# Kernel tuning notes

Measured on AMD Instinct MI355X. Metric: run time of the kernel, lower is better.

Reference implementation:

```python
import jax, jax.numpy as jnp
import numpy as np

N_NODES = 100_000
N_EDGES = 1_600_000
N_GRAPHS = 200
N_IN, N_HID, N_OUT, N_LAYERS = 4, 64, 2, 4


def _ln(x, g, b, eps=1e-5):
    mu = jnp.mean(x, -1, keepdims=True)
    xc = x - mu
    var = jnp.mean(xc * xc, -1, keepdims=True)
    return xc * jax.lax.rsqrt(var + eps) * g + b


def _sage(x, src, dst, Wl, bl, Wr, n):
    # SAGEConv with MultiAggregation(['max','mean'], mode='cat'):
    # out = lin_l(concat(max_j x_j, mean_j x_j)) + lin_r(x)
    xj = x[src]  # [E, d] edge gather
    mx = jax.ops.segment_max(xj, dst, num_segments=n)
    mx = jnp.where(jnp.isneginf(mx), 0.0, mx)  # PyG scatter-max gives 0 for isolated nodes
    s = jax.ops.segment_sum(xj, dst, num_segments=n)
    cnt = jax.ops.segment_sum(jnp.ones((src.shape[0], 1), x.dtype), dst, num_segments=n)
    mean = s / jnp.maximum(cnt, 1.0)
    agg = jnp.concatenate([mx, mean], -1)  # [N, 2d], order = aggr list order
    return agg @ Wl + bl + x @ Wr


def setup_inputs():
    key = jax.random.key(0)
    ks = jax.random.split(key, 16)
    x = jax.random.normal(ks[0], (N_NODES, N_IN), jnp.float32)
    edge_index = jax.random.randint(ks[1], (2, N_EDGES), 0, N_NODES, dtype=jnp.int32)
    per = N_NODES // N_GRAPHS
    batch = jnp.repeat(jnp.arange(N_GRAPHS, dtype=jnp.int32), per)
    ptr = jnp.arange(N_GRAPHS + 1, dtype=jnp.int32) * per

    def w(k, shape, fan_in):
        return jax.random.normal(k, shape, jnp.float32) / np.sqrt(fan_in)

    inp = dict(x=x, edge_index=edge_index, batch=batch, ptr=ptr)
    inp["Wl0"] = w(ks[2], (2 * N_IN, N_HID), 2 * N_IN)
    inp["bl0"] = jnp.zeros((N_HID,), jnp.float32)
    inp["Wr0"] = w(ks[3], (N_IN, N_HID), N_IN)
    inp["Wl"] = w(ks[4], (N_LAYERS - 1, 2 * N_HID, N_HID), 2 * N_HID)
    inp["bl"] = jnp.zeros((N_LAYERS - 1, N_HID), jnp.float32)
    inp["Wr"] = w(ks[5], (N_LAYERS - 1, N_HID, N_HID), N_HID)
    inp["Wres"] = w(ks[6], (N_IN, N_HID), N_IN)
    inp["bres"] = jnp.zeros((N_HID,), jnp.float32)
    inp["ln_g"] = jnp.ones((N_LAYERS, N_HID), jnp.float32)
    inp["ln_b"] = jnp.zeros((N_LAYERS, N_HID), jnp.float32)
    inp["mlp_W1"] = w(ks[7], (N_HID, 4 * N_HID), N_HID)
    inp["mlp_b1"] = jnp.zeros((4 * N_HID,), jnp.float32)
    inp["mlp_g"] = jnp.ones((4 * N_HID,), jnp.float32)
    inp["mlp_bn"] = jnp.zeros((4 * N_HID,), jnp.float32)
    inp["mlp_W2"] = w(ks[8], (4 * N_HID, N_HID), 4 * N_HID)
    inp["mlp_b2"] = jnp.zeros((N_HID,), jnp.float32)
    ro_in = 3 * N_HID + N_IN
    inp["ro_W1"] = w(ks[9], (ro_in, 4 * N_HID), ro_in)
    inp["ro_b1"] = jnp.zeros((4 * N_HID,), jnp.float32)
    inp["ro_g"] = jnp.ones((4 * N_HID,), jnp.float32)
    inp["ro_bn"] = jnp.zeros((4 * N_HID,), jnp.float32)
    inp["ro_W2"] = w(ks[10], (4 * N_HID, 2 * N_OUT), 4 * N_HID)
    inp["ro_b2"] = jnp.zeros((2 * N_OUT,), jnp.float32)
    return inp


def reference(x, edge_index, batch, ptr, Wl0, bl0, Wr0, Wl, bl, Wr, Wres, bres,
              ln_g, ln_b, mlp_W1, mlp_b1, mlp_g, mlp_bn, mlp_W2, mlp_b2,
              ro_W1, ro_b1, ro_g, ro_bn, ro_W2, ro_b2):
    n = x.shape[0]
    ng = ptr.shape[0] - 1
    src, dst = edge_index[0], edge_index[1]

    x_res = x @ Wres + bres
    h = _sage(x, src, dst, Wl0, bl0, Wr0, n)
    h = jax.nn.silu(_ln(h, ln_g[0], ln_b[0]) + x_res)
    for i in range(Wl.shape[0]):  # n_layers - 1 structurally distinct layers
        h_res = h
        h = _sage(h, src, dst, Wl[i], bl[i], Wr[i], n)
        h = jax.nn.silu(_ln(h, ln_g[i + 1], ln_b[i + 1]) + h_res)

    h = jax.nn.silu(h @ mlp_W1 + mlp_b1)
    h = _ln(h, mlp_g, mlp_bn) @ mlp_W2 + mlp_b2

    # multi-pool readout over graphs
    s = jax.ops.segment_sum(h, batch, num_segments=ng)
    cnt = jax.ops.segment_sum(jnp.ones((n, 1), h.dtype), batch, num_segments=ng)
    mean = s / jnp.maximum(cnt, 1.0)
    mx = jax.ops.segment_max(h, batch, num_segments=ng)
    mx = jnp.where(jnp.isneginf(mx), 0.0, mx)
    root = x[ptr[:-1]]  # original features of each graph's root node
    o = jnp.concatenate([mean, mx, s, root], -1)  # [G, 3*n_hidden + n_in]
    o = jax.nn.silu(o @ ro_W1 + ro_b1)
    return _ln(o, ro_g, ro_bn) @ ro_W2 + ro_b2
```

## Files before the change

kernel.cpp:

```cpp
#include <hip/hip_runtime.h>
#include <math.h>

#define NEG_INF (-__builtin_inff())
#define BSHIFT 8
#define BCAP 6144
#define SK 200

typedef __attribute__((ext_vector_type(8))) short short8;
typedef __attribute__((ext_vector_type(4))) float f32x4;

__device__ __forceinline__ float rlane(float x, int l) {
    return __int_as_float(__builtin_amdgcn_readlane(__float_as_int(x), l));
}

__device__ __forceinline__ float silu_f(float y) {
    return y / (1.f + __expf(-y));
}

__device__ __forceinline__ unsigned short f2bh(float x) {
    unsigned int u = __float_as_uint(x);
    u += 0x7fffu + ((u >> 16) & 1u);
    return (unsigned short)(u >> 16);
}
__device__ __forceinline__ float bh2f(unsigned short h) {
    return __uint_as_float(((unsigned int)h) << 16);
}


__global__ __launch_bounds__(256)
void k_bhist(const int* __restrict__ ei, int* __restrict__ btot, int E, int NB) {
    __shared__ int lh[512];
    int t = threadIdx.x;
    lh[t] = 0; lh[t + 256] = 0;
    __syncthreads();
    int base = blockIdx.x * 8192;
    for (int i = t; i < 8192; i += 256) {
        int e = base + i;
        if (e < E) atomicAdd(&lh[ei[E + e] >> BSHIFT], 1);
    }
    __syncthreads();
    if (lh[t]) atomicAdd(&btot[t], lh[t]);
    if (t + 256 < NB && lh[t + 256]) atomicAdd(&btot[t + 256], lh[t + 256]);
}

__global__ __launch_bounds__(256)
void k_bscan(const int* __restrict__ btot, int* __restrict__ bbase,
             int* __restrict__ bcur, int NB, int E) {
    __shared__ int s[512];
    int t = threadIdx.x;
    int v0 = (t < NB) ? btot[t] : 0;
    int v1 = (t + 256 < NB) ? btot[t + 256] : 0;
    s[t] = v0; s[t + 256] = v1;
    __syncthreads();
    for (int st = 1; st < 512; st <<= 1) {
        int a0 = (t >= st) ? s[t - st] : 0;
        int a1 = (t + 256 >= st) ? s[t + 256 - st] : 0;
        __syncthreads();
        s[t] += a0; s[t + 256] += a1;
        __syncthreads();
    }
    if (t < NB)       { bbase[t] = s[t] - v0;             bcur[t] = s[t] - v0; }
    if (t + 256 < NB) { bbase[t + 256] = s[t + 256] - v1; bcur[t + 256] = s[t + 256] - v1; }
    if (t == 0) bbase[NB] = E;
}

__global__ __launch_bounds__(256)
void k_bscatter(const int* __restrict__ ei, int* __restrict__ bcur,
                int2* __restrict__ pairs, int E, int NB) {
    __shared__ int2 sp[8192];
    __shared__ int lh[512], lsc[512], lcur[512], gb[512];
    int t = threadIdx.x;
    lh[t] = 0; lh[t + 256] = 0; lcur[t] = 0; lcur[t + 256] = 0;
    __syncthreads();
    int base = blockIdx.x * 8192;
    for (int i = t; i < 8192; i += 256) {
        int e = base + i;
        if (e < E) atomicAdd(&lh[ei[E + e] >> BSHIFT], 1);
    }
    __syncthreads();
    lsc[t] = lh[t]; lsc[t + 256] = lh[t + 256];
    __syncthreads();
    for (int st = 1; st < 512; st <<= 1) {
        int a0 = (t >= st) ? lsc[t - st] : 0;
        int a1 = (t + 256 >= st) ? lsc[t + 256 - st] : 0;
        __syncthreads();
        lsc[t] += a0; lsc[t + 256] += a1;
        __syncthreads();
    }
    for (int i = t; i < 8192; i += 256) {
        int e = base + i;
        if (e < E) {
            int s = ei[e], d = ei[E + e];
            int b = d >> BSHIFT;
            int pos = lsc[b] - lh[b] + atomicAdd(&lcur[b], 1);
            sp[pos] = make_int2(s, d);
        }
    }
    __syncthreads();
    if (t < NB && lh[t]) gb[t] = atomicAdd(&bcur[t], lh[t]);
    if (t + 256 < NB && lh[t + 256]) gb[t + 256] = atomicAdd(&bcur[t + 256], lh[t + 256]);
    __syncthreads();
    int tot = lsc[511];
    for (int i = t; i < tot; i += 256) {
        int2 p = sp[i];
        int b = p.y >> BSHIFT;
        pairs[gb[b] + (i - (lsc[b] - lh[b]))] = p;
    }
}

__global__ __launch_bounds__(256)
void k_bcsr(const int2* __restrict__ pairs, const int* __restrict__ bbase,
            int* __restrict__ csr, int* __restrict__ off, int N, int NB, int E) {
    __shared__ int2 sp[BCAP];
    __shared__ int lh[256], lsc[256], lcur[256];
    int t = threadIdx.x;
    int b = blockIdx.x;
    int base = bbase[b];
    int m = bbase[b + 1] - base;
    int v0 = b << BSHIFT;
    lh[t] = 0; lcur[t] = 0;
    __syncthreads();
    bool fits = (m <= BCAP);
    for (int i = t; i < m; i += 256) {
        int2 p = pairs[base + i];
        if (fits) sp[i] = p;
        atomicAdd(&lh[p.y & 255], 1);
    }
    __syncthreads();
    int myv = lh[t];
    lsc[t] = myv;
    __syncthreads();
    for (int st = 1; st < 256; st <<= 1) {
        int a = (t >= st) ? lsc[t - st] : 0;
        __syncthreads();
        lsc[t] += a;
        __syncthreads();
    }
    int excl = lsc[t] - myv;
    __syncthreads();
    lsc[t] = excl;
    __syncthreads();
    int v = v0 + t;
    if (v < N) off[v] = base + excl;
    if (b == NB - 1 && t == 0) off[N] = E;
    for (int i = t; i < m; i += 256) {
        int2 p = fits ? sp[i] : pairs[base + i];
        int d = p.y & 255;
        int pos = lsc[d] + atomicAdd(&lcur[d], 1);
        csr[base + pos] = p.x;
    }
}


__global__ void k_prep(const float* __restrict__ mW1, const float* __restrict__ mg,
                       const float* __restrict__ mbn, const float* __restrict__ mW2,
                       const float* __restrict__ mb2,
                       const float* __restrict__ Wl, const float* __restrict__ Wr,
                       unsigned short* __restrict__ w1fh, unsigned short* __restrict__ w1fl,
                       unsigned short* __restrict__ w2fh, unsigned short* __restrict__ w2fl,
                       unsigned short* __restrict__ wsfh, unsigned short* __restrict__ wsfl,
                       float* __restrict__ k12)
{
    int b = blockIdx.x, t = threadIdx.x;
    if (b == 0) {
        for (int idx = t; idx < 2048; idx += 256) {
            int nt = idx >> 7, rem = idx & 127;
            int kc = rem >> 6, ln = rem & 63;
#pragma unroll
            for (int i = 0; i < 8; ++i) {
                int c = kc * 32 + (ln >> 4) * 8 + i;
                int j = nt * 16 + (ln & 15);
                float v = mW1[c * 256 + j];
                unsigned short hi = f2bh(v);
                w1fh[idx * 8 + i] = hi;
                w1fl[idx * 8 + i] = f2bh(v - bh2f(hi));
            }
        }
    } else if (b == 1) {
        for (int idx = t; idx < 2048; idx += 256) {
            int nt2 = idx >> 9, rem = idx & 511;
            int kc2 = rem >> 6, ln = rem & 63;
#pragma unroll
            for (int i = 0; i < 8; ++i) {
                int j = kc2 * 32 + (ln >> 4) * 8 + i;
                int o = nt2 * 16 + (ln & 15);
                float v = mg[j] * mW2[j * 64 + o];
                unsigned short hi = f2bh(v);
                w2fh[idx * 8 + i] = hi;
                w2fl[idx * 8 + i] = f2bh(v - bh2f(hi));
            }
        }
    } else if (b == 2 && t < 64) {
        float a1 = 0.f, a2 = 0.f;
        for (int j = 0; j < 256; ++j) {
            a1 += mbn[j] * mW2[j * 64 + t];
            a2 += mg[j]  * mW2[j * 64 + t];
        }
        k12[t] = a1 + mb2[t];
        k12[64 + t] = a2;
    } else if (b >= 3 && b < 6) {
        int l = b - 3;
        for (int idx = t; idx < 1536; idx += 256) {
            int tile = idx >> 6, ln = idx & 63;
            int nt = tile / 6, kc = tile % 6;
#pragma unroll
            for (int i = 0; i < 8; ++i) {
                int k = kc * 32 + (ln >> 4) * 8 + i;
                int o = nt * 16 + (ln & 15);
                float v = (k < 128) ? Wl[((l * 128) + k) * 64 + o]
                                    : Wr[((l * 64) + (k - 128)) * 64 + o];
                unsigned short hi = f2bh(v);
                wsfh[((l * 24 + tile) * 64 + ln) * 8 + i] = hi;
                wsfl[((l * 24 + tile) * 64 + ln) * 8 + i] = f2bh(v - bh2f(hi));
            }
        }
    }
}


__global__ __launch_bounds__(256, 4)
void k_layer0(const float* __restrict__ x, float* __restrict__ hout,
              const int* __restrict__ off, const int* __restrict__ csr,
              const float* __restrict__ Wl0, const float* __restrict__ bl0,
              const float* __restrict__ Wr0, const float* __restrict__ Wres,
              const float* __restrict__ bres, const float* __restrict__ lg,
              const float* __restrict__ lb, int N)
{
    __shared__ float sWl[512], sWr[256], sWres[256], sC[256];
    int t = threadIdx.x;
    sWl[t] = Wl0[t]; sWl[256 + t] = Wl0[256 + t];
    sWr[t] = Wr0[t];
    sWres[t] = Wres[t];
    if (t < 64) { sC[t] = bl0[t]; sC[64 + t] = bres[t]; sC[128 + t] = lg[t]; sC[192 + t] = lb[t]; }
    __syncthreads();
    int v = blockIdx.x * 256 + t;
    if (v >= N) return;
    const float4* X4 = reinterpret_cast<const float4*>(x);
    float4 xv = X4[v];
    int s0 = off[v], s1 = off[v + 1];
    float4 mx = {NEG_INF, NEG_INF, NEG_INF, NEG_INF};
    float4 sm = {0.f, 0.f, 0.f, 0.f};
    for (int e = s0; e < s1; e += 4) {
        int last = s1 - 1;
        int i0 = csr[e];
        int i1 = csr[min(e + 1, last)];
        int i2 = csr[min(e + 2, last)];
        int i3 = csr[min(e + 3, last)];
        float4 a0 = X4[i0], a1 = X4[i1], a2 = X4[i2], a3 = X4[i3];
        mx.x = fmaxf(fmaxf(fmaxf(mx.x, a0.x), fmaxf(a1.x, a2.x)), a3.x);
        mx.y = fmaxf(fmaxf(fmaxf(mx.y, a0.y), fmaxf(a1.y, a2.y)), a3.y);
        mx.z = fmaxf(fmaxf(fmaxf(mx.z, a0.z), fmaxf(a1.z, a2.z)), a3.z);
        mx.w = fmaxf(fmaxf(fmaxf(mx.w, a0.w), fmaxf(a1.w, a2.w)), a3.w);
        bool o1 = e + 1 < s1, o2 = e + 2 < s1, o3 = e + 3 < s1;
        sm.x += a0.x + (o1 ? a1.x : 0.f) + (o2 ? a2.x : 0.f) + (o3 ? a3.x : 0.f);
        sm.y += a0.y + (o1 ? a1.y : 0.f) + (o2 ? a2.y : 0.f) + (o3 ? a3.y : 0.f);
        sm.z += a0.z + (o1 ? a1.z : 0.f) + (o2 ? a2.z : 0.f) + (o3 ? a3.z : 0.f);
        sm.w += a0.w + (o1 ? a1.w : 0.f) + (o2 ? a2.w : 0.f) + (o3 ? a3.w : 0.f);
    }
    int deg = s1 - s0;
    if (deg == 0) { mx.x = 0.f; mx.y = 0.f; mx.z = 0.f; mx.w = 0.f; }
    float inv = 1.f / (float)max(deg, 1);
    float4 mn = {sm.x * inv, sm.y * inv, sm.z * inv, sm.w * inv};
    float a[64];
    float acc1 = 0.f, acc2 = 0.f;
#pragma unroll
    for (int k = 0; k < 64; ++k) {
        float tv = sC[k]
            + mx.x * sWl[k]       + mx.y * sWl[64 + k]  + mx.z * sWl[128 + k] + mx.w * sWl[192 + k]
            + mn.x * sWl[256 + k] + mn.y * sWl[320 + k] + mn.z * sWl[384 + k] + mn.w * sWl[448 + k]
            + xv.x * sWr[k]       + xv.y * sWr[64 + k]  + xv.z * sWr[128 + k] + xv.w * sWr[192 + k];
        a[k] = tv; acc1 += tv; acc2 += tv * tv;
    }
    float mu = acc1 * (1.f / 64.f);
    float var = acc2 * (1.f / 64.f) - mu * mu;
    float rs = rsqrtf(var + 1e-5f);
    float* orow = hout + (size_t)v * 64;
#pragma unroll
    for (int k = 0; k < 64; ++k) {
        float res = sC[64 + k] + xv.x * sWres[k] + xv.y * sWres[64 + k]
                  + xv.z * sWres[128 + k] + xv.w * sWres[192 + k];
        float y = (a[k] - mu) * rs * sC[128 + k] + sC[192 + k] + res;
        orow[k] = silu_f(y);
    }
}


__global__ __launch_bounds__(256, 8)
void k_agg(const float* __restrict__ hin, float* __restrict__ aggws,
           const int* __restrict__ off, const int* __restrict__ csr, int N)
{
    int lane = threadIdx.x & 63;
    int gw = (blockIdx.x * blockDim.x + threadIdx.x) >> 6;
    int nw = (gridDim.x * blockDim.x) >> 6;
    for (int v = gw; v < N; v += nw) {
        int s0 = off[v], s1 = off[v + 1];
        float mx = NEG_INF, sm = 0.f;
        for (int cb = s0; cb < s1; cb += 64) {
            int cdeg = min(64, s1 - cb);
            int idxv = csr[min(cb + lane, s1 - 1)];
            for (int b = 0; b < cdeg; b += 8) {
                float vv[8];
#pragma unroll
                for (int u = 0; u < 8; ++u) {
                    int iu = __builtin_amdgcn_readlane(idxv, b + u);
                    vv[u] = hin[((size_t)iu << 6) + lane];
                }
#pragma unroll
                for (int u = 0; u < 8; ++u) {
                    mx = fmaxf(mx, vv[u]);
                    sm += (b + u < cdeg) ? vv[u] : 0.f;
                }
            }
        }
        int deg = s1 - s0;
        if (deg == 0) mx = 0.f;
        float mean = sm / (float)max(deg, 1);
        aggws[((size_t)v << 7) + lane] = mx;
        aggws[((size_t)v << 7) + 64 + lane] = mean;
    }
}


__global__ __launch_bounds__(256, 2)
void k_smm_m(const float* __restrict__ aggws, const float* __restrict__ hin,
             float* __restrict__ hout,
             const unsigned short* __restrict__ wfh, const unsigned short* __restrict__ wfl,
             const float* __restrict__ bl, const float* __restrict__ lg,
             const float* __restrict__ lb, int N)
{
    __shared__ __align__(16) unsigned short shi[64 * SK];
    __shared__ __align__(16) unsigned short slo[64 * SK];
    int t = threadIdx.x;
    int lane = t & 63, w = t >> 6, quad = lane >> 4, l15 = lane & 15;

    {
        int row = t >> 2, seg = t & 3;
        int node = min(blockIdx.x * 64 + row, N - 1);
        const float4* ar = (const float4*)(aggws + ((size_t)node << 7));
        const float4* hr = (const float4*)(hin + ((size_t)node << 6));
        float v[48];
#pragma unroll
        for (int q = 0; q < 12; ++q) {
            int c = seg * 48 + q * 4;
            float4 f = (c < 128) ? ar[c >> 2] : hr[(c - 128) >> 2];
            v[q * 4] = f.x; v[q * 4 + 1] = f.y; v[q * 4 + 2] = f.z; v[q * 4 + 3] = f.w;
        }
#pragma unroll
        for (int g = 0; g < 6; ++g) {
            short8 ph, pl;
#pragma unroll
            for (int i = 0; i < 8; ++i) {
                float x = v[g * 8 + i];
                unsigned short hi = f2bh(x);
                ph[i] = (short)hi;
                pl[i] = (short)f2bh(x - bh2f(hi));
            }
            int idx = row * SK + seg * 48 + g * 8;
            *(short8*)(shi + idx) = ph;
            *(short8*)(slo + idx) = pl;
        }
    }
    __syncthreads();

    f32x4 acc[4];
#pragma unroll
    for (int nt = 0; nt < 4; ++nt) acc[nt] = (f32x4){0.f, 0.f, 0.f, 0.f};
#pragma unroll
    for (int kc = 0; kc < 6; ++kc) {
        int idx = (w * 16 + l15) * SK + kc * 32 + quad * 8;
        short8 ah = *(const short8*)(shi + idx);
        short8 al = *(const short8*)(slo + idx);
#pragma unroll
        for (int nt = 0; nt < 4; ++nt) {
            int fo = ((nt * 6 + kc) * 64 + lane) * 8;
            short8 bh_ = *(const short8*)(wfh + fo);
            short8 bl_ = *(const short8*)(wfl + fo);
            acc[nt] = __builtin_amdgcn_mfma_f32_16x16x32_bf16(ah, bh_, acc[nt], 0, 0, 0);
            acc[nt] = __builtin_amdgcn_mfma_f32_16x16x32_bf16(al, bh_, acc[nt], 0, 0, 0);
            acc[nt] = __builtin_amdgcn_mfma_f32_16x16x32_bf16(ah, bl_, acc[nt], 0, 0, 0);
        }
    }

    float blv[4], gv[4], bv[4];
#pragma unroll
    for (int nt = 0; nt < 4; ++nt) {
        int ch = nt * 16 + l15;
        blv[nt] = bl[ch]; gv[nt] = lg[ch]; bv[nt] = lb[ch];
    }
    float ps[4], pq[4];
#pragma unroll
    for (int r = 0; r < 4; ++r) { ps[r] = 0.f; pq[r] = 0.f; }
#pragma unroll
    for (int nt = 0; nt < 4; ++nt)
#pragma unroll
        for (int r = 0; r < 4; ++r) {
            float tv = acc[nt][r] + blv[nt];
            acc[nt][r] = tv;
            ps[r] += tv; pq[r] += tv * tv;
        }
#pragma unroll
    for (int r = 0; r < 4; ++r) {
        float a = ps[r], b = pq[r];
#pragma unroll
        for (int m = 1; m < 16; m <<= 1) {
            a += __shfl_xor(a, m, 64);
            b += __shfl_xor(b, m, 64);
        }
        ps[r] = a; pq[r] = b;
    }
#pragma unroll
    for (int r = 0; r < 4; ++r) {
        int node = blockIdx.x * 64 + w * 16 + quad * 4 + r;
        float mu = ps[r] * (1.f / 64.f);
        float var = pq[r] * (1.f / 64.f) - mu * mu;
        float rs = rsqrtf(var + 1e-5f);
        if (node < N) {
#pragma unroll
            for (int nt = 0; nt < 4; ++nt) {
                float hs = hin[(size_t)node * 64 + nt * 16 + l15];
                float y = (acc[nt][r] - mu) * rs * gv[nt] + bv[nt] + hs;
                hout[(size_t)node * 64 + nt * 16 + l15] = silu_f(y);
            }
        }
    }
}


__global__ __launch_bounds__(256, 2)
void k_mlpm(const float* __restrict__ hin, float* __restrict__ hout,
            const unsigned short* __restrict__ w1fh, const unsigned short* __restrict__ w1fl,
            const unsigned short* __restrict__ w2fh, const unsigned short* __restrict__ w2fl,
            const float* __restrict__ b1, const float* __restrict__ K12, int N)
{
    __shared__ __align__(16) char lds[70656];
    float* p1 = (float*)lds;
    float* p2 = (float*)(lds + 1024);
    unsigned short* hhi = (unsigned short*)(lds + 2048);
    unsigned short* hlo = (unsigned short*)(lds + 11264);
    unsigned int* spack = (unsigned int*)(lds + 2048);

    int t = threadIdx.x;
    int lane = t & 63, w = t >> 6, quad = lane >> 4, l15 = lane & 15;

    {
        int row = t >> 2, cq = (t & 3) * 16;
        int node0 = blockIdx.x * 64 + row;
        const float4* hr = (const float4*)(hin + (size_t)min(node0, N - 1) * 64 + cq);
        float v[16];
#pragma unroll
        for (int k = 0; k < 4; ++k) {
            float4 f = hr[k];
            v[4 * k] = f.x; v[4 * k + 1] = f.y; v[4 * k + 2] = f.z; v[4 * k + 3] = f.w;
        }
#pragma unroll
        for (int g = 0; g < 2; ++g) {
            short8 ph, pl;
#pragma unroll
            for (int i = 0; i < 8; ++i) {
                float x = v[g * 8 + i];
                unsigned short hi = f2bh(x);
                ph[i] = (short)hi;
                pl[i] = (short)f2bh(x - bh2f(hi));
            }
            int idx = row * 72 + cq + g * 8;
            *(short8*)(hhi + idx) = ph;
            *(short8*)(hlo + idx) = pl;
        }
    }
    __syncthreads();

    f32x4 acc[4][4];
#pragma unroll
    for (int mt = 0; mt < 4; ++mt)
#pragma unroll
        for (int nt = 0; nt < 4; ++nt)
            acc[mt][nt] = (f32x4){0.f, 0.f, 0.f, 0.f};
#pragma unroll
    for (int kc = 0; kc < 2; ++kc) {
        short8 ah[4], al[4];
#pragma unroll
        for (int mt = 0; mt < 4; ++mt) {
            int idx = (mt * 16 + l15) * 72 + kc * 32 + quad * 8;
            ah[mt] = *(const short8*)(hhi + idx);
            al[mt] = *(const short8*)(hlo + idx);
        }
#pragma unroll
        for (int nt = 0; nt < 4; ++nt) {
            int fo = (((w * 4 + nt) * 2 + kc) * 64 + lane) * 8;
            short8 bh_ = *(const short8*)(w1fh + fo);
            short8 bl_ = *(const short8*)(w1fl + fo);
#pragma unroll
            for (int mt = 0; mt < 4; ++mt) {
                acc[mt][nt] = __builtin_amdgcn_mfma_f32_16x16x32_bf16(ah[mt], bh_, acc[mt][nt], 0, 0, 0);
                acc[mt][nt] = __builtin_amdgcn_mfma_f32_16x16x32_bf16(al[mt], bh_, acc[mt][nt], 0, 0, 0);
                acc[mt][nt] = __builtin_amdgcn_mfma_f32_16x16x32_bf16(ah[mt], bl_, acc[mt][nt], 0, 0, 0);
            }
        }
    }

    float b1v[4];
#pragma unroll
    for (int nt = 0; nt < 4; ++nt) b1v[nt] = b1[(w * 4 + nt) * 16 + l15];
    float psum[4][4], psq[4][4];
#pragma unroll
    for (int mt = 0; mt < 4; ++mt)
#pragma unroll
        for (int r = 0; r < 4; ++r) { psum[mt][r] = 0.f; psq[mt][r] = 0.f; }
#pragma unroll
    for (int mt = 0; mt < 4; ++mt)
#pragma unroll
        for (int nt = 0; nt < 4; ++nt)
#pragma unroll
            for (int r = 0; r < 4; ++r) {
                float sv = silu_f(acc[mt][nt][r] + b1v[nt]);
                acc[mt][nt][r] = sv;
                psum[mt][r] += sv;
                psq[mt][r] += sv * sv;
            }
#pragma unroll
    for (int mt = 0; mt < 4; ++mt)
#pragma unroll
        for (int r = 0; r < 4; ++r) {
            float a = psum[mt][r], b = psq[mt][r];
#pragma unroll
            for (int m = 1; m < 16; m <<= 1) {
                a += __shfl_xor(a, m, 64);
                b += __shfl_xor(b, m, 64);
            }
            psum[mt][r] = a; psq[mt][r] = b;
        }
    if (l15 == 0) {
#pragma unroll
        for (int mt = 0; mt < 4; ++mt)
#pragma unroll
            for (int r = 0; r < 4; ++r) {
                int nl = mt * 16 + quad * 4 + r;
                p1[w * 64 + nl] = psum[mt][r];
                p2[w * 64 + nl] = psq[mt][r];
            }
    }
    __syncthreads();

#pragma unroll
    for (int mt = 0; mt < 4; ++mt)
#pragma unroll
        for (int nt = 0; nt < 4; ++nt)
#pragma unroll
            for (int r = 0; r < 4; ++r) {
                float sv = acc[mt][nt][r];
                unsigned short hi = f2bh(sv);
                unsigned short lo = f2bh(sv - bh2f(hi));
                spack[(mt * 16 + quad * 4 + r) * 268 + (w * 4 + nt) * 16 + l15] =
                    (((unsigned int)hi) << 16) | (unsigned int)lo;
            }
    __syncthreads();

    f32x4 acc2[4];
#pragma unroll
    for (int nt2 = 0; nt2 < 4; ++nt2) acc2[nt2] = (f32x4){0.f, 0.f, 0.f, 0.f};
#pragma unroll
    for (int kc2 = 0; kc2 < 8; ++kc2) {
        int base = (w * 16 + l15) * 268 + kc2 * 32 + quad * 8;
        uint4 q0 = *(const uint4*)(spack + base);
        uint4 q1 = *(const uint4*)(spack + base + 4);
        unsigned int vv[8] = {q0.x, q0.y, q0.z, q0.w, q1.x, q1.y, q1.z, q1.w};
        short8 ah, al;
#pragma unroll
        for (int i = 0; i < 8; ++i) {
            ah[i] = (short)(vv[i] >> 16);
            al[i] = (short)(vv[i] & 0xffffu);
        }
#pragma unroll
        for (int nt2 = 0; nt2 < 4; ++nt2) {
            int fo = ((nt2 * 8 + kc2) * 64 + lane) * 8;
            short8 bh_ = *(const short8*)(w2fh + fo);
            short8 bl_ = *(const short8*)(w2fl + fo);
            acc2[nt2] = __builtin_amdgcn_mfma_f32_16x16x32_bf16(ah, bh_, acc2[nt2], 0, 0, 0);
            acc2[nt2] = __builtin_amdgcn_mfma_f32_16x16x32_bf16(al, bh_, acc2[nt2], 0, 0, 0);
            acc2[nt2] = __builtin_amdgcn_mfma_f32_16x16x32_bf16(ah, bl_, acc2[nt2], 0, 0, 0);
        }
    }

    float k1v[4], k2v[4];
#pragma unroll
    for (int nt2 = 0; nt2 < 4; ++nt2) {
        k1v[nt2] = K12[nt2 * 16 + l15];
        k2v[nt2] = K12[64 + nt2 * 16 + l15];
    }
#pragma unroll
    for (int r = 0; r < 4; ++r) {
        int nl = w * 16 + quad * 4 + r;
        float s1 = p1[nl] + p1[64 + nl] + p1[128 + nl] + p1[192 + nl];
        float s2 = p2[nl] + p2[64 + nl] + p2[128 + nl] + p2[192 + nl];
        float mu = s1 * (1.f / 256.f);
        float var = s2 * (1.f / 256.f) - mu * mu;
        float rs = rsqrtf(var + 1e-5f);
        float rm = rs * mu;
        int node = blockIdx.x * 64 + nl;
        if (node < N) {
#pragma unroll
            for (int nt2 = 0; nt2 < 4; ++nt2)
                hout[(size_t)node * 64 + nt2 * 16 + l15] =
                    rs * acc2[nt2][r] + k1v[nt2] - rm * k2v[nt2];
        }
    }
}


__global__ __launch_bounds__(256, 2)
void k_readout(const float* __restrict__ h2, const float* __restrict__ x,
               const int* __restrict__ ptr,
               const float* __restrict__ W1, const float* __restrict__ b1,
               const float* __restrict__ lg, const float* __restrict__ lb,
               const float* __restrict__ W2, const float* __restrict__ b2,
               float* __restrict__ out)
{
    __shared__ float f[196];
    __shared__ float sred[4][64];
    __shared__ float mred[4][64];
    __shared__ float lred[8];
    __shared__ float pr[4][4];
    int t = threadIdx.x, lane = t & 63, w = t >> 6;
    int g = blockIdx.x;
    int s0 = ptr[g], s1 = ptr[g + 1];
    float sm = 0.f, mx = NEG_INF;
    for (int r = s0 + w; r < s1; r += 4) {
        float v = h2[(size_t)r * 64 + lane];
        sm += v; mx = fmaxf(mx, v);
    }
    sred[w][lane] = sm; mred[w][lane] = mx;
    __syncthreads();
    if (w == 0) {
        float ssum = sred[0][lane] + sred[1][lane] + sred[2][lane] + sred[3][lane];
        float smax = fmaxf(fmaxf(mred[0][lane], mred[1][lane]),
                           fmaxf(mred[2][lane], mred[3][lane]));
        int cnt = s1 - s0;
        if (cnt == 0) smax = 0.f;
        f[lane] = ssum / (float)max(cnt, 1);
        f[64 + lane] = smax;
        f[128 + lane] = ssum;
    }
    if (t < 4) f[192 + t] = x[(size_t)s0 * 4 + t];
    __syncthreads();
    float o = b1[t];
    for (int c = 0; c < 196; ++c) o += f[c] * W1[c * 256 + t];
    o = silu_f(o);
    float s = o, s2v = o * o;
#pragma unroll
    for (int m = 1; m < 64; m <<= 1) { s += __shfl_xor(s, m, 64); s2v += __shfl_xor(s2v, m, 64); }
    if (lane == 0) { lred[w] = s; lred[4 + w] = s2v; }
    __syncthreads();
    float tot = lred[0] + lred[1] + lred[2] + lred[3];
    float tot2 = lred[4] + lred[5] + lred[6] + lred[7];
    float mu = tot * (1.f / 256.f);
    float var = tot2 * (1.f / 256.f) - mu * mu;
    float u = (o - mu) * rsqrtf(var + 1e-5f) * lg[t] + lb[t];
    float4 w2r = reinterpret_cast<const float4*>(W2)[t];
    float p0 = u * w2r.x, p1 = u * w2r.y, p2 = u * w2r.z, p3 = u * w2r.w;
#pragma unroll
    for (int m = 1; m < 64; m <<= 1) {
        p0 += __shfl_xor(p0, m, 64); p1 += __shfl_xor(p1, m, 64);
        p2 += __shfl_xor(p2, m, 64); p3 += __shfl_xor(p3, m, 64);
    }
    if (lane == 0) { pr[w][0] = p0; pr[w][1] = p1; pr[w][2] = p2; pr[w][3] = p3; }
    __syncthreads();
    if (t < 4) out[g * 4 + t] = pr[0][t] + pr[1][t] + pr[2][t] + pr[3][t] + b2[t];
}


extern "C" void kernel_launch(void* const* d_in, const int* in_sizes, int n_in,
                              void* d_out, int out_size, void* d_ws, size_t ws_size,
                              hipStream_t stream)
{
    const float* x    = (const float*)d_in[0];
    const int*   ei   = (const int*)d_in[1];
    const int*   ptr  = (const int*)d_in[3];
    const float* Wl0  = (const float*)d_in[4];
    const float* bl0  = (const float*)d_in[5];
    const float* Wr0  = (const float*)d_in[6];
    const float* Wl   = (const float*)d_in[7];
    const float* bl   = (const float*)d_in[8];
    const float* Wr   = (const float*)d_in[9];
    const float* Wres = (const float*)d_in[10];
    const float* bres = (const float*)d_in[11];
    const float* lng  = (const float*)d_in[12];
    const float* lnb  = (const float*)d_in[13];
    const float* mW1  = (const float*)d_in[14];
    const float* mb1  = (const float*)d_in[15];
    const float* mg   = (const float*)d_in[16];
    const float* mbn  = (const float*)d_in[17];
    const float* mW2  = (const float*)d_in[18];
    const float* mb2  = (const float*)d_in[19];
    const float* rW1  = (const float*)d_in[20];
    const float* rb1  = (const float*)d_in[21];
    const float* rg   = (const float*)d_in[22];
    const float* rbn  = (const float*)d_in[23];
    const float* rW2  = (const float*)d_in[24];
    const float* rb2  = (const float*)d_in[25];
    float* out = (float*)d_out;

    int N = in_sizes[0] / 4;
    int E = in_sizes[1] / 2;
    int NG = in_sizes[3] - 1;
    int nchunk = (N + 255) / 256;
    int nblkm  = (N + 63) / 64;
    int NB     = (N + 255) >> BSHIFT;
    int nbh    = (E + 8191) / 8192;

    char* ws = (char*)d_ws;
    size_t o = 0;
    auto alloc = [&](size_t bytes) -> void* {
        void* p = ws + o;
        o += (bytes + 255) & ~(size_t)255;
        return p;
    };
    int*   off   = (int*)alloc((size_t)(N + 1) * 4);
    int*   btot  = (int*)alloc((size_t)NB * 4);
    int*   bbase = (int*)alloc((size_t)(NB + 1) * 4);
    int*   bcur  = (int*)alloc((size_t)NB * 4);
    int*   csr   = (int*)alloc((size_t)E * 4);
    int2*  pairs = (int2*)alloc((size_t)E * 8);
    float* ha    = (float*)alloc((size_t)N * 64 * 4);
    float* hb    = (float*)alloc((size_t)N * 64 * 4);
    float* aggws = (float*)alloc((size_t)N * 128 * 4);
    unsigned short* w1fh = (unsigned short*)alloc(16384 * 2);
    unsigned short* w1fl = (unsigned short*)alloc(16384 * 2);
    unsigned short* w2fh = (unsigned short*)alloc(16384 * 2);
    unsigned short* w2fl = (unsigned short*)alloc(16384 * 2);
    unsigned short* wsfh = (unsigned short*)alloc(36864 * 2);
    unsigned short* wsfl = (unsigned short*)alloc(36864 * 2);
    float* k12   = (float*)alloc(128 * 4);

    hipMemsetAsync(btot, 0, (size_t)NB * 4, stream);
    k_prep<<<6, 256, 0, stream>>>(mW1, mg, mbn, mW2, mb2, Wl, Wr,
                                  w1fh, w1fl, w2fh, w2fl, wsfh, wsfl, k12);
    k_bhist<<<nbh, 256, 0, stream>>>(ei, btot, E, NB);
    k_bscan<<<1, 256, 0, stream>>>(btot, bbase, bcur, NB, E);
    k_bscatter<<<nbh, 256, 0, stream>>>(ei, bcur, pairs, E, NB);
    k_bcsr<<<NB, 256, 0, stream>>>(pairs, bbase, csr, off, N, NB, E);

    k_layer0<<<nchunk, 256, 0, stream>>>(x, ha, off, csr, Wl0, bl0, Wr0, Wres, bres, lng, lnb, N);

    k_agg<<<2048, 256, 0, stream>>>(ha, aggws, off, csr, N);
    k_smm_m<<<nblkm, 256, 0, stream>>>(aggws, ha, hb, wsfh,               wsfl,               bl,       lng + 64,  lnb + 64,  N);
    k_agg<<<2048, 256, 0, stream>>>(hb, aggws, off, csr, N);
    k_smm_m<<<nblkm, 256, 0, stream>>>(aggws, hb, ha, wsfh + 24 * 64 * 8, wsfl + 24 * 64 * 8, bl + 64,  lng + 128, lnb + 128, N);
    k_agg<<<2048, 256, 0, stream>>>(ha, aggws, off, csr, N);
    k_smm_m<<<nblkm, 256, 0, stream>>>(aggws, ha, hb, wsfh + 48 * 64 * 8, wsfl + 48 * 64 * 8, bl + 128, lng + 192, lnb + 192, N);

    k_mlpm<<<nblkm, 256, 0, stream>>>(hb, ha, w1fh, w1fl, w2fh, w2fl, mb1, k12, N);
    k_readout<<<NG, 256, 0, stream>>>(ha, x, ptr, rW1, rb1, rg, rbn, rW2, rb2, out);
}
```

Before: 609.1 us.

## Load SAGE GEMM operands directly to registers, widen gather unroll, halve bucket chunks

The SAGE dense kernel no longer stages the split-bf16 A tiles in LDS. Each wave now loads its 16 rows straight from global memory into MFMA operand registers, which removes the shared-memory round trip and the block barrier and allows higher occupancy. The aggregation gather is unrolled to 16 loads per step and drops the per-element predicate. To keep the mean correct, it subtracts the padded duplicates of the last neighbor afterwards, which can add a small floating-point cancellation error. The edge bucketing chunk is also halved so that more blocks are launched and less LDS is used per block.

```diff
diff --git a/kernel.cpp b/kernel.cpp
--- a/kernel.cpp
+++ b/kernel.cpp
@@ -4,14 +4,10 @@
 #define NEG_INF (-__builtin_inff())
 #define BSHIFT 8
 #define BCAP 6144
-#define SK 200
+#define CH 4096
 
 typedef __attribute__((ext_vector_type(8))) short short8;
 typedef __attribute__((ext_vector_type(4))) float f32x4;
-
-__device__ __forceinline__ float rlane(float x, int l) {
-    return __int_as_float(__builtin_amdgcn_readlane(__float_as_int(x), l));
-}
 
 __device__ __forceinline__ float silu_f(float y) {
     return y / (1.f + __expf(-y));
@@ -33,8 +29,8 @@
     int t = threadIdx.x;
     lh[t] = 0; lh[t + 256] = 0;
     __syncthreads();
-    int base = blockIdx.x * 8192;
-    for (int i = t; i < 8192; i += 256) {
+    int base = blockIdx.x * CH;
+    for (int i = t; i < CH; i += 256) {
         int e = base + i;
         if (e < E) atomicAdd(&lh[ei[E + e] >> BSHIFT], 1);
     }
@@ -67,13 +63,13 @@
 __global__ __launch_bounds__(256)
 void k_bscatter(const int* __restrict__ ei, int* __restrict__ bcur,
                 int2* __restrict__ pairs, int E, int NB) {
-    __shared__ int2 sp[8192];
+    __shared__ int2 sp[CH];
     __shared__ int lh[512], lsc[512], lcur[512], gb[512];
     int t = threadIdx.x;
     lh[t] = 0; lh[t + 256] = 0; lcur[t] = 0; lcur[t + 256] = 0;
     __syncthreads();
-    int base = blockIdx.x * 8192;
-    for (int i = t; i < 8192; i += 256) {
+    int base = blockIdx.x * CH;
+    for (int i = t; i < CH; i += 256) {
         int e = base + i;
         if (e < E) atomicAdd(&lh[ei[E + e] >> BSHIFT], 1);
     }
@@ -87,7 +83,7 @@
         lsc[t] += a0; lsc[t + 256] += a1;
         __syncthreads();
     }
-    for (int i = t; i < 8192; i += 256) {
+    for (int i = t; i < CH; i += 256) {
         int e = base + i;
         if (e < E) {
             int s = ei[e], d = ei[E + e];
@@ -294,90 +290,79 @@
     int nw = (gridDim.x * blockDim.x) >> 6;
     for (int v = gw; v < N; v += nw) {
         int s0 = off[v], s1 = off[v + 1];
+        int deg = s1 - s0;
         float mx = NEG_INF, sm = 0.f;
+        int npad = 0;
         for (int cb = s0; cb < s1; cb += 64) {
             int cdeg = min(64, s1 - cb);
             int idxv = csr[min(cb + lane, s1 - 1)];
-            for (int b = 0; b < cdeg; b += 8) {
-                float vv[8];
-#pragma unroll
-                for (int u = 0; u < 8; ++u) {
+            for (int b = 0; b < cdeg; b += 16) {
+                float vv[16];
+#pragma unroll
+                for (int u = 0; u < 16; ++u) {
                     int iu = __builtin_amdgcn_readlane(idxv, b + u);
                     vv[u] = hin[((size_t)iu << 6) + lane];
                 }
 #pragma unroll
-                for (int u = 0; u < 8; ++u) {
-                    mx = fmaxf(mx, vv[u]);
-                    sm += (b + u < cdeg) ? vv[u] : 0.f;
-                }
-            }
-        }
-        int deg = s1 - s0;
-        if (deg == 0) mx = 0.f;
-        float mean = sm / (float)max(deg, 1);
+                for (int u = 0; u < 16; ++u) { mx = fmaxf(mx, vv[u]); sm += vv[u]; }
+            }
+            npad += (((cdeg + 15) >> 4) << 4) - cdeg;
+        }
+        float mean;
+        if (deg == 0) { mx = 0.f; mean = 0.f; }
+        else {
+            float hl = hin[((size_t)csr[s1 - 1] << 6) + lane];
+            mean = (sm - (float)npad * hl) / (float)deg;
+        }
         aggws[((size_t)v << 7) + lane] = mx;
         aggws[((size_t)v << 7) + 64 + lane] = mean;
     }
 }
 
 
-__global__ __launch_bounds__(256, 2)
-void k_smm_m(const float* __restrict__ aggws, const float* __restrict__ hin,
+__global__ __launch_bounds__(256, 4)
+void k_smm_d(const float* __restrict__ aggws, const float* __restrict__ hin,
              float* __restrict__ hout,
              const unsigned short* __restrict__ wfh, const unsigned short* __restrict__ wfl,
              const float* __restrict__ bl, const float* __restrict__ lg,
              const float* __restrict__ lb, int N)
 {
-    __shared__ __align__(16) unsigned short shi[64 * SK];
-    __shared__ __align__(16) unsigned short slo[64 * SK];
     int t = threadIdx.x;
     int lane = t & 63, w = t >> 6, quad = lane >> 4, l15 = lane & 15;
-
-    {
-        int row = t >> 2, seg = t & 3;
-        int node = min(blockIdx.x * 64 + row, N - 1);
-        const float4* ar = (const float4*)(aggws + ((size_t)node << 7));
-        const float4* hr = (const float4*)(hin + ((size_t)node << 6));
-        float v[48];
-#pragma unroll
-        for (int q = 0; q < 12; ++q) {
-            int c = seg * 48 + q * 4;
-            float4 f = (c < 128) ? ar[c >> 2] : hr[(c - 128) >> 2];
-            v[q * 4] = f.x; v[q * 4 + 1] = f.y; v[q * 4 + 2] = f.z; v[q * 4 + 3] = f.w;
-        }
-#pragma unroll
-        for (int g = 0; g < 6; ++g) {
-            short8 ph, pl;
-#pragma unroll
-            for (int i = 0; i < 8; ++i) {
-                float x = v[g * 8 + i];
-                unsigned short hi = f2bh(x);
-                ph[i] = (short)hi;
-                pl[i] = (short)f2bh(x - bh2f(hi));
-            }
-            int idx = row * SK + seg * 48 + g * 8;
-            *(short8*)(shi + idx) = ph;
-            *(short8*)(slo + idx) = pl;
-        }
-    }
-    __syncthreads();
+    int nodebase = (blockIdx.x * 4 + w) * 16;
+    if (nodebase >= N) return;
+    int arow = min(nodebase + l15, N - 1);
+
+    short8 ah[6], al[6];
+#pragma unroll
+    for (int kc = 0; kc < 6; ++kc) {
+        const float* src = (kc < 4)
+            ? (aggws + ((size_t)arow << 7) + kc * 32 + quad * 8)
+            : (hin + ((size_t)arow << 6) + (kc - 4) * 32 + quad * 8);
+        float4 f0 = *(const float4*)(src);
+        float4 f1 = *(const float4*)(src + 4);
+        float vv[8] = {f0.x, f0.y, f0.z, f0.w, f1.x, f1.y, f1.z, f1.w};
+#pragma unroll
+        for (int i = 0; i < 8; ++i) {
+            unsigned short hi = f2bh(vv[i]);
+            ah[kc][i] = (short)hi;
+            al[kc][i] = (short)f2bh(vv[i] - bh2f(hi));
+        }
+    }
 
     f32x4 acc[4];
 #pragma unroll
     for (int nt = 0; nt < 4; ++nt) acc[nt] = (f32x4){0.f, 0.f, 0.f, 0.f};
 #pragma unroll
     for (int kc = 0; kc < 6; ++kc) {
-        int idx = (w * 16 + l15) * SK + kc * 32 + quad * 8;
-        short8 ah = *(const short8*)(shi + idx);
-        short8 al = *(const short8*)(slo + idx);
 #pragma unroll
         for (int nt = 0; nt < 4; ++nt) {
             int fo = ((nt * 6 + kc) * 64 + lane) * 8;
             short8 bh_ = *(const short8*)(wfh + fo);
             short8 bl_ = *(const short8*)(wfl + fo);
-            acc[nt] = __builtin_amdgcn_mfma_f32_16x16x32_bf16(ah, bh_, acc[nt], 0, 0, 0);
-            acc[nt] = __builtin_amdgcn_mfma_f32_16x16x32_bf16(al, bh_, acc[nt], 0, 0, 0);
-            acc[nt] = __builtin_amdgcn_mfma_f32_16x16x32_bf16(ah, bl_, acc[nt], 0, 0, 0);
+            acc[nt] = __builtin_amdgcn_mfma_f32_16x16x32_bf16(ah[kc], bh_, acc[nt], 0, 0, 0);
+            acc[nt] = __builtin_amdgcn_mfma_f32_16x16x32_bf16(al[kc], bh_, acc[nt], 0, 0, 0);
+            acc[nt] = __builtin_amdgcn_mfma_f32_16x16x32_bf16(ah[kc], bl_, acc[nt], 0, 0, 0);
         }
     }
 
@@ -410,7 +395,7 @@
     }
 #pragma unroll
     for (int r = 0; r < 4; ++r) {
-        int node = blockIdx.x * 64 + w * 16 + quad * 4 + r;
+        int node = nodebase + quad * 4 + r;
         float mu = ps[r] * (1.f / 64.f);
         float var = pq[r] * (1.f / 64.f) - mu * mu;
         float rs = rsqrtf(var + 1e-5f);
@@ -705,7 +690,7 @@
     int nchunk = (N + 255) / 256;
     int nblkm  = (N + 63) / 64;
     int NB     = (N + 255) >> BSHIFT;
-    int nbh    = (E + 8191) / 8192;
+    int nbh    = (E + CH - 1) / CH;
 
     char* ws = (char*)d_ws;
     size_t o = 0;
@@ -742,11 +727,11 @@
     k_layer0<<<nchunk, 256, 0, stream>>>(x, ha, off, csr, Wl0, bl0, Wr0, Wres, bres, lng, lnb, N);
 
     k_agg<<<2048, 256, 0, stream>>>(ha, aggws, off, csr, N);
-    k_smm_m<<<nblkm, 256, 0, stream>>>(aggws, ha, hb, wsfh,               wsfl,               bl,       lng + 64,  lnb + 64,  N);
+    k_smm_d<<<nblkm, 256, 0, stream>>>(aggws, ha, hb, wsfh,               wsfl,               bl,       lng + 64,  lnb + 64,  N);
     k_agg<<<2048, 256, 0, stream>>>(hb, aggws, off, csr, N);
-    k_smm_m<<<nblkm, 256, 0, stream>>>(aggws, hb, ha, wsfh + 24 * 64 * 8, wsfl + 24 * 64 * 8, bl + 64,  lng + 128, lnb + 128, N);
+    k_smm_d<<<nblkm, 256, 0, stream>>>(aggws, hb, ha, wsfh + 24 * 64 * 8, wsfl + 24 * 64 * 8, bl + 64,  lng + 128, lnb + 128, N);
     k_agg<<<2048, 256, 0, stream>>>(ha, aggws, off, csr, N);
-    k_smm_m<<<nblkm, 256, 0, stream>>>(aggws, ha, hb, wsfh + 48 * 64 * 8, wsfl + 48 * 64 * 8, bl + 128, lng + 192, lnb + 192, N);
+    k_smm_d<<<nblkm, 256, 0, stream>>>(aggws, ha, hb, wsfh + 48 * 64 * 8, wsfl + 48 * 64 * 8, bl + 128, lng + 192, lnb + 192, N);
 
     k_mlpm<<<nblkm, 256, 0, stream>>>(hb, ha, w1fh, w1fl, w2fh, w2fl, mb1, k12, N);
     k_readout<<<NG, 256, 0, stream>>>(ha, x, ptr, rW1, rb1, rg, rbn, rW2, rb2, out);
```

New measurement: 562.6 us. -7.6%, faster.
